# Kernel optimization log

Measured on AMD Instinct MI355X. Metric: run time of the kernel, lower is better.

## Reference

```python
import jax, jax.numpy as jnp
import numpy as np

B, S, T, D = 4, 512, 512, 256


def setup_inputs() -> dict:
    key = jax.random.key(0)
    ks = jax.random.split(key, 10)
    scale = 1.0 / np.sqrt(D)
    return {
        "source": jax.random.normal(ks[0], (B, S, D), jnp.float32),
        "target": jax.random.normal(ks[1], (B, T, D), jnp.float32),
        "W_src": jax.random.uniform(ks[2], (D, D), jnp.float32, -scale, scale),
        "b_src": jax.random.uniform(ks[3], (D,), jnp.float32, -scale, scale),
        "W_tgt": jax.random.uniform(ks[4], (D, D), jnp.float32, -scale, scale),
        "b_tgt": jax.random.uniform(ks[5], (D,), jnp.float32, -scale, scale),
        "W_res": jax.random.uniform(ks[6], (D, 1), jnp.float32, -scale, scale),
        "b_res": jax.random.uniform(ks[7], (1,), jnp.float32, -scale, scale),
        "W_prob": jax.random.uniform(ks[8], (D, 2), jnp.float32, -scale, scale),
        "b_prob": jax.random.uniform(ks[9], (2,), jnp.float32, -scale, scale),
    }


def reference(source, target, W_src, b_src, W_tgt, b_tgt, W_res, b_res, W_prob, b_prob):
    # source: (B,S,D), target: (B,T,D)
    src_lin = jnp.einsum("bsd,de->bse", source, W_src) + b_src  # (B,S,D)
    tgt_lin = jnp.einsum("btd,de->bte", target, W_tgt) + b_tgt  # (B,T,D)
    # Bahdanau-style additive attention: (B,T,S,D) broadcast, tanh, D->1
    h = jnp.tanh(src_lin[:, None, :, :] + tgt_lin[:, :, None, :])  # (B,T,S,D)
    genP = jnp.einsum("btsd,d->bts", h, W_res[:, 0]) + b_res[0]     # (B,T,S)
    prob = jax.nn.softmax(jnp.einsum("btd,de->bte", target, W_prob) + b_prob, axis=-1)  # (B,T,2)
    return genP, prob
```

## Files before the change

### kernel.cpp

```cpp
#include <hip/hip_runtime.h>

#define B_ 4
#define S_ 512
#define T_ 512
#define D_ 256
#define NSRC (B_ * S_)
#define NROW 4096
#define K2F 2.8853900817779268f

typedef __attribute__((ext_vector_type(8))) short short8;
typedef __attribute__((ext_vector_type(4))) float f32x4;
typedef __attribute__((ext_vector_type(2))) float f32x2;

__device__ __forceinline__ unsigned short f2bf(float f) {
    union { float f; unsigned u; } v; v.f = f;
    unsigned r = v.u + 0x7FFF + ((v.u >> 16) & 1);
    return (unsigned short)(r >> 16);
}

__global__ __launch_bounds__(256) void ysyt_kernel(
    const float* __restrict__ src, const float* __restrict__ tgt,
    const float* __restrict__ Wsrc, const float* __restrict__ Wtgt,
    const float* __restrict__ Wp,  const float* __restrict__ bp,
    const float* __restrict__ bsrc, const float* __restrict__ btgt,
    float* __restrict__ yst, float* __restrict__ out)
{
    __shared__ unsigned short lwt[16384];
    const int bid = blockIdx.x, tid = threadIdx.x;
    const int lane = tid & 63, w = tid >> 6;

    if (bid < 256) {
        const int rowblk = bid >> 2, colq = bid & 3;
        const int R0 = rowblk * 64;
        const int n = lane & 15, quad = lane >> 4;
        const int mat = (R0 >= NSRC) ? 1 : 0;
        const float* bias = mat ? btgt : bsrc;
        const float* Wm = mat ? Wtgt : Wsrc;
        const float* xb = mat ? &tgt[(R0 - NSRC) * D_] : &src[R0 * D_];

        {
            const int r = tid;
            const int ksr = r >> 5, qr = (r >> 3) & 3, jr = r & 7;
            const int wbase = ksr * 512 + qr * 8 + jr;
            #pragma unroll 4
            for (int i = 0; i < 16; i++) {
                float4 v = *(const float4*)&Wm[r * D_ + colq * 64 + 4 * i];
                const int cc = 4 * i;
                lwt[((cc + 0) >> 4) * 4096 + ((cc + 0) & 15) * 32 + wbase] = f2bf(v.x);
                lwt[((cc + 1) >> 4) * 4096 + ((cc + 1) & 15) * 32 + wbase] = f2bf(v.y);
                lwt[((cc + 2) >> 4) * 4096 + ((cc + 2) & 15) * 32 + wbase] = f2bf(v.z);
                lwt[((cc + 3) >> 4) * 4096 + ((cc + 3) & 15) * 32 + wbase] = f2bf(v.w);
            }
        }

        short8 af[8];
        #pragma unroll
        for (int ks = 0; ks < 8; ks++) {
            const float* p = &xb[(w * 16 + n) * D_ + ks * 32 + quad * 8];
            float4 u0 = *(const float4*)p;
            float4 u1 = *(const float4*)(p + 4);
            short8 v;
            v[0] = (short)f2bf(u0.x); v[1] = (short)f2bf(u0.y);
            v[2] = (short)f2bf(u0.z); v[3] = (short)f2bf(u0.w);
            v[4] = (short)f2bf(u1.x); v[5] = (short)f2bf(u1.y);
            v[6] = (short)f2bf(u1.z); v[7] = (short)f2bf(u1.w);
            af[ks] = v;
        }
        __syncthreads();

        #pragma unroll
        for (int gc = 0; gc < 4; gc++) {
            const int gcol = colq * 4 + gc;
            const unsigned short* bp2 = &lwt[gc * 4096 + n * 32 + quad * 8];
            short8 bf[8];
            #pragma unroll
            for (int ks = 0; ks < 8; ks++) bf[ks] = *(const short8*)&bp2[ks * 512];
            f32x4 a4 = {0.f, 0.f, 0.f, 0.f};
            #pragma unroll
            for (int ks = 0; ks < 8; ks++)
                a4 = __builtin_amdgcn_mfma_f32_16x16x32_bf16(af[ks], bf[ks], a4, 0, 0, 0);
            const float bv = bias[gcol * 16 + n];
            float4 o;
            o.x = __builtin_amdgcn_exp2f((a4[0] + bv) * K2F);
            o.y = __builtin_amdgcn_exp2f((a4[1] + bv) * K2F);
            o.z = __builtin_amdgcn_exp2f((a4[2] + bv) * K2F);
            o.w = __builtin_amdgcn_exp2f((a4[3] + bv) * K2F);
            *(float4*)&yst[(gcol * 16 + n) * NROW + R0 + w * 16 + quad * 4] = o;
        }
    } else {
        int row  = (bid - 256) * 4 + w;
        float p0 = 0.f, p1 = 0.f;
        #pragma unroll
        for (int i = 0; i < 4; i++) {
            int d = lane + i * 64;
            float v = tgt[row * D_ + d];
            float2 wv = *(const float2*)&Wp[d * 2];
            p0 = fmaf(v, wv.x, p0);
            p1 = fmaf(v, wv.y, p1);
        }
        #pragma unroll
        for (int off = 32; off > 0; off >>= 1) {
            p0 += __shfl_down(p0, off, 64);
            p1 += __shfl_down(p1, off, 64);
        }
        if (lane == 0) {
            const float L2E = 1.4426950408889634f;
            float l0 = p0 + bp[0], l1 = p1 + bp[1];
            float e10 = __builtin_amdgcn_exp2f((l1 - l0) * L2E);
            float e01 = __builtin_amdgcn_exp2f((l0 - l1) * L2E);
            out[B_ * T_ * S_ + row * 2 + 0] = __builtin_amdgcn_rcpf(1.f + e10);
            out[B_ * T_ * S_ + row * 2 + 1] = __builtin_amdgcn_rcpf(1.f + e01);
        }
    }
}

__global__ __launch_bounds__(256) void genp_kernel(
    const float* __restrict__ yst,
    const float* __restrict__ Wres, const float* __restrict__ bres,
    float* __restrict__ out)
{
    const int tid = threadIdx.x;
    const int lane = tid & 63;
    const int s0 = blockIdx.x * 64;
    const int t0 = blockIdx.y * 32;
    const int b  = blockIdx.z >> 1;
    const int dh = blockIdx.z & 1;
    const int m  = tid & 15;
    const int g  = tid >> 4;

    const int scol = b * S_ + s0 + 4 * m;
    const int tcol = NSRC + b * T_ + t0 + 2 * g;
    const int dbase = dh * 128;

    f32x2 acc[2][2];
    acc[0][0] = (f32x2){0.f, 0.f}; acc[0][1] = (f32x2){0.f, 0.f};
    acc[1][0] = (f32x2){0.f, 0.f}; acc[1][1] = (f32x2){0.f, 0.f};
    const f32x2 one2 = {1.f, 1.f};

    #define KQLOAD(AS, AT, DQ) do {                                          \
        _Pragma("unroll")                                                    \
        for (int k = 0; k < 4; k++) {                                        \
            AS[k] = *(const float4*)&yst[(size_t)((DQ) + k) * NROW + scol];  \
            AT[k] = *(const float2*)&yst[(size_t)((DQ) + k) * NROW + tcol];  \
        }                                                                    \
    } while (0)

    #define KQBODY(AS, AT, DQ) do {                                          \
        const float w0 = Wres[(DQ) + 0], w1 = Wres[(DQ) + 1];                \
        const float w2 = Wres[(DQ) + 2], w3 = Wres[(DQ) + 3];                \
        const f32x2 wv0 = {w0, w0}, wv1 = {w1, w1};                          \
        const f32x2 wv2 = {w2, w2}, wv3 = {w3, w3};                          \
        _Pragma("unroll")                                                    \
        for (int i = 0; i < 2; i++) {                                        \
            const float c0 = i ? AT[0].y : AT[0].x;                          \
            const float c1 = i ? AT[1].y : AT[1].x;                          \
            const float c2 = i ? AT[2].y : AT[2].x;                          \
            const float c3 = i ? AT[3].y : AT[3].x;                          \
            const f32x2 c0v = {c0, c0}, c1v = {c1, c1};                      \
            const f32x2 c2v = {c2, c2}, c3v = {c3, c3};                      \
            _Pragma("unroll")                                                \
            for (int jp = 0; jp < 2; jp++) {                                 \
                const f32x2 a0 = jp ? (f32x2){AS[0].z, AS[0].w}              \
                                    : (f32x2){AS[0].x, AS[0].y};             \
                const f32x2 a1 = jp ? (f32x2){AS[1].z, AS[1].w}              \
                                    : (f32x2){AS[1].x, AS[1].y};             \
                const f32x2 a2 = jp ? (f32x2){AS[2].z, AS[2].w}              \
                                    : (f32x2){AS[2].x, AS[2].y};             \
                const f32x2 a3 = jp ? (f32x2){AS[3].z, AS[3].w}              \
                                    : (f32x2){AS[3].x, AS[3].y};             \
                f32x2 dd0 = a0 * c0v + one2;                                 \
                f32x2 dd1 = a1 * c1v + one2;                                 \
                f32x2 dd2 = a2 * c2v + one2;                                 \
                f32x2 dd3 = a3 * c3v + one2;                                 \
                f32x2 p01 = dd0 * dd1;                                       \
                f32x2 p23 = dd2 * dd3;                                       \
                f32x2 den = p01 * p23;                                       \
                f32x2 u01 = dd1 * wv0; u01 = dd0 * wv1 + u01;                \
                f32x2 u23 = dd3 * wv2; u23 = dd2 * wv3 + u23;                \
                f32x2 num = u01 * p23; num = u23 * p01 + num;                \
                f32x2 r;                                                     \
                r.x = __builtin_amdgcn_rcpf(den.x);                          \
                r.y = __builtin_amdgcn_rcpf(den.y);                          \
                acc[i][jp] = num * r + acc[i][jp];                           \
            }                                                                \
        }                                                                    \
    } while (0)

    float4 sA[4], sB[4];
    float2 tA[4], tB[4];
    KQLOAD(sA, tA, dbase);
    for (int it = 0; it < 16; it++) {
        const int dq = dbase + it * 8;
        KQLOAD(sB, tB, dq + 4);
        KQBODY(sA, tA, dq);
        if (it < 15) KQLOAD(sA, tA, dq + 8);
        KQBODY(sB, tB, dq + 4);
    }
    #undef KQLOAD
    #undef KQBODY

    float cw = Wres[lane] + Wres[lane + 64] + Wres[lane + 128] + Wres[lane + 192];
    #pragma unroll
    for (int off = 32; off > 0; off >>= 1) cw += __shfl_xor(cw, off, 64);
    const float C0 = (dh == 0) ? (cw + bres[0]) : 0.f;

    #pragma unroll
    for (int i = 0; i < 2; i++) {
        float* orow = &out[(size_t)(b * T_ + t0 + 2 * g + i) * S_ + s0 + 4 * m];
        #pragma unroll
        for (int jp = 0; jp < 2; jp++) {
            unsafeAtomicAdd(&orow[2 * jp + 0], C0 - 2.f * acc[i][jp].x);
            unsafeAtomicAdd(&orow[2 * jp + 1], C0 - 2.f * acc[i][jp].y);
        }
    }
}

extern "C" void kernel_launch(void* const* d_in, const int* in_sizes, int n_in,
                              void* d_out, int out_size, void* d_ws, size_t ws_size,
                              hipStream_t stream) {
    const float* source = (const float*)d_in[0];
    const float* target = (const float*)d_in[1];
    const float* W_src  = (const float*)d_in[2];
    const float* b_src  = (const float*)d_in[3];
    const float* W_tgt  = (const float*)d_in[4];
    const float* b_tgt  = (const float*)d_in[5];
    const float* W_res  = (const float*)d_in[6];
    const float* b_res  = (const float*)d_in[7];
    const float* W_prob = (const float*)d_in[8];
    const float* b_prob = (const float*)d_in[9];
    float* out = (float*)d_out;

    float* yst = (float*)d_ws;

    ysyt_kernel<<<768, 256, 0, stream>>>(source, target, W_src, W_tgt,
                                         W_prob, b_prob, b_src, b_tgt,
                                         yst, out);
    genp_kernel<<<dim3(8, 16, 8), 256, 0, stream>>>(yst, W_res, b_res, out);
}
```

Measured before the change: 130.2 us.

## Stage ys/yt tiles in LDS and enlarge per-thread output tile in genp

genp_kernel now loads 64x64 slices of the source and target projections into shared memory once per block and computes a 4x4 output tile per thread from LDS. The d dimension is split four ways instead of two, and the t tile grows to 64. This targets repeated global/L2 reads of the projection data and raises arithmetic per load. In exchange it doubles the number of atomic adds to the output and adds a block-level barrier and LDS traffic.

```diff
diff --git a/kernel.cpp b/kernel.cpp
--- a/kernel.cpp
+++ b/kernel.cpp
@@ -119,55 +119,70 @@
     const float* __restrict__ Wres, const float* __restrict__ bres,
     float* __restrict__ out)
 {
+    __shared__ float lys[64][68];
+    __shared__ float lyt[64][68];
+
     const int tid = threadIdx.x;
     const int lane = tid & 63;
     const int s0 = blockIdx.x * 64;
-    const int t0 = blockIdx.y * 32;
-    const int b  = blockIdx.z >> 1;
-    const int dh = blockIdx.z & 1;
+    const int t0 = blockIdx.y * 64;
+    const int b  = blockIdx.z >> 2;
+    const int dq = blockIdx.z & 3;
+    const int d0 = dq * 64;
     const int m  = tid & 15;
     const int g  = tid >> 4;
 
-    const int scol = b * S_ + s0 + 4 * m;
-    const int tcol = NSRC + b * T_ + t0 + 2 * g;
-    const int dbase = dh * 128;
-
-    f32x2 acc[2][2];
-    acc[0][0] = (f32x2){0.f, 0.f}; acc[0][1] = (f32x2){0.f, 0.f};
-    acc[1][0] = (f32x2){0.f, 0.f}; acc[1][1] = (f32x2){0.f, 0.f};
+    {
+        const int r = tid >> 2, q = tid & 3;
+        const int sbase = b * S_ + s0;
+        const int tbase = NSRC + b * T_ + t0;
+        #pragma unroll
+        for (int j = 0; j < 4; j++) {
+            float4 vs = *(const float4*)&yst[(size_t)(d0 + r) * NROW + sbase + q * 16 + 4 * j];
+            float4 vt = *(const float4*)&yst[(size_t)(d0 + r) * NROW + tbase + q * 16 + 4 * j];
+            *(float4*)&lys[r][q * 16 + 4 * j] = vs;
+            *(float4*)&lyt[r][q * 16 + 4 * j] = vt;
+        }
+    }
+    __syncthreads();
+
+    f32x2 acc[4][2];
+    #pragma unroll
+    for (int i = 0; i < 4; i++) {
+        acc[i][0] = (f32x2){0.f, 0.f};
+        acc[i][1] = (f32x2){0.f, 0.f};
+    }
     const f32x2 one2 = {1.f, 1.f};
 
-    #define KQLOAD(AS, AT, DQ) do {                                          \
-        _Pragma("unroll")                                                    \
-        for (int k = 0; k < 4; k++) {                                        \
-            AS[k] = *(const float4*)&yst[(size_t)((DQ) + k) * NROW + scol];  \
-            AT[k] = *(const float2*)&yst[(size_t)((DQ) + k) * NROW + tcol];  \
-        }                                                                    \
-    } while (0)
-
-    #define KQBODY(AS, AT, DQ) do {                                          \
-        const float w0 = Wres[(DQ) + 0], w1 = Wres[(DQ) + 1];                \
-        const float w2 = Wres[(DQ) + 2], w3 = Wres[(DQ) + 3];                \
-        const f32x2 wv0 = {w0, w0}, wv1 = {w1, w1};                          \
-        const f32x2 wv2 = {w2, w2}, wv3 = {w3, w3};                          \
-        _Pragma("unroll")                                                    \
-        for (int i = 0; i < 2; i++) {                                        \
-            const float c0 = i ? AT[0].y : AT[0].x;                          \
-            const float c1 = i ? AT[1].y : AT[1].x;                          \
-            const float c2 = i ? AT[2].y : AT[2].x;                          \
-            const float c3 = i ? AT[3].y : AT[3].x;                          \
-            const f32x2 c0v = {c0, c0}, c1v = {c1, c1};                      \
-            const f32x2 c2v = {c2, c2}, c3v = {c3, c3};                      \
+    #pragma unroll 4
+    for (int kq = 0; kq < 16; kq++) {
+        const int dk = 4 * kq;
+        float4 sA[4], tA[4];
+        #pragma unroll
+        for (int k = 0; k < 4; k++) {
+            sA[k] = *(const float4*)&lys[dk + k][4 * m];
+            tA[k] = *(const float4*)&lyt[dk + k][4 * g];
+        }
+        const float w0 = Wres[d0 + dk + 0], w1 = Wres[d0 + dk + 1];
+        const float w2 = Wres[d0 + dk + 2], w3 = Wres[d0 + dk + 3];
+        const f32x2 wv0 = {w0, w0}, wv1 = {w1, w1};
+        const f32x2 wv2 = {w2, w2}, wv3 = {w3, w3};
+
+        #define FOLD(TT, COMP) {                                             \
+            const f32x2 c0v = {tA[0].COMP, tA[0].COMP};                      \
+            const f32x2 c1v = {tA[1].COMP, tA[1].COMP};                      \
+            const f32x2 c2v = {tA[2].COMP, tA[2].COMP};                      \
+            const f32x2 c3v = {tA[3].COMP, tA[3].COMP};                      \
             _Pragma("unroll")                                                \
             for (int jp = 0; jp < 2; jp++) {                                 \
-                const f32x2 a0 = jp ? (f32x2){AS[0].z, AS[0].w}              \
-                                    : (f32x2){AS[0].x, AS[0].y};             \
-                const f32x2 a1 = jp ? (f32x2){AS[1].z, AS[1].w}              \
-                                    : (f32x2){AS[1].x, AS[1].y};             \
-                const f32x2 a2 = jp ? (f32x2){AS[2].z, AS[2].w}              \
-                                    : (f32x2){AS[2].x, AS[2].y};             \
-                const f32x2 a3 = jp ? (f32x2){AS[3].z, AS[3].w}              \
-                                    : (f32x2){AS[3].x, AS[3].y};             \
+                const f32x2 a0 = jp ? (f32x2){sA[0].z, sA[0].w}              \
+                                    : (f32x2){sA[0].x, sA[0].y};             \
+                const f32x2 a1 = jp ? (f32x2){sA[1].z, sA[1].w}              \
+                                    : (f32x2){sA[1].x, sA[1].y};             \
+                const f32x2 a2 = jp ? (f32x2){sA[2].z, sA[2].w}              \
+                                    : (f32x2){sA[2].x, sA[2].y};             \
+                const f32x2 a3 = jp ? (f32x2){sA[3].z, sA[3].w}              \
+                                    : (f32x2){sA[3].x, sA[3].y};             \
                 f32x2 dd0 = a0 * c0v + one2;                                 \
                 f32x2 dd1 = a1 * c1v + one2;                                 \
                 f32x2 dd2 = a2 * c2v + one2;                                 \
@@ -181,37 +196,25 @@
                 f32x2 r;                                                     \
                 r.x = __builtin_amdgcn_rcpf(den.x);                          \
                 r.y = __builtin_amdgcn_rcpf(den.y);                          \
-                acc[i][jp] = num * r + acc[i][jp];                           \
+                acc[TT][jp] = num * r + acc[TT][jp];                         \
             }                                                                \
-        }                                                                    \
-    } while (0)
-
-    float4 sA[4], sB[4];
-    float2 tA[4], tB[4];
-    KQLOAD(sA, tA, dbase);
-    for (int it = 0; it < 16; it++) {
-        const int dq = dbase + it * 8;
-        KQLOAD(sB, tB, dq + 4);
-        KQBODY(sA, tA, dq);
-        if (it < 15) KQLOAD(sA, tA, dq + 8);
-        KQBODY(sB, tB, dq + 4);
-    }
-    #undef KQLOAD
-    #undef KQBODY
+        }
+        FOLD(0, x) FOLD(1, y) FOLD(2, z) FOLD(3, w)
+        #undef FOLD
+    }
 
     float cw = Wres[lane] + Wres[lane + 64] + Wres[lane + 128] + Wres[lane + 192];
     #pragma unroll
     for (int off = 32; off > 0; off >>= 1) cw += __shfl_xor(cw, off, 64);
-    const float C0 = (dh == 0) ? (cw + bres[0]) : 0.f;
+    const float C0 = (dq == 0) ? (cw + bres[0]) : 0.f;
 
     #pragma unroll
-    for (int i = 0; i < 2; i++) {
-        float* orow = &out[(size_t)(b * T_ + t0 + 2 * g + i) * S_ + s0 + 4 * m];
-        #pragma unroll
-        for (int jp = 0; jp < 2; jp++) {
-            unsafeAtomicAdd(&orow[2 * jp + 0], C0 - 2.f * acc[i][jp].x);
-            unsafeAtomicAdd(&orow[2 * jp + 1], C0 - 2.f * acc[i][jp].y);
-        }
+    for (int i = 0; i < 4; i++) {
+        float* orow = &out[(size_t)(b * T_ + t0 + 4 * g + i) * S_ + s0 + 4 * m];
+        unsafeAtomicAdd(&orow[0], C0 - 2.f * acc[i][0].x);
+        unsafeAtomicAdd(&orow[1], C0 - 2.f * acc[i][0].y);
+        unsafeAtomicAdd(&orow[2], C0 - 2.f * acc[i][1].x);
+        unsafeAtomicAdd(&orow[3], C0 - 2.f * acc[i][1].y);
     }
 }
 
@@ -235,5 +238,5 @@
     ysyt_kernel<<<768, 256, 0, stream>>>(source, target, W_src, W_tgt,
                                          W_prob, b_prob, b_src, b_tgt,
                                          yst, out);
-    genp_kernel<<<dim3(8, 16, 8), 256, 0, stream>>>(yst, W_res, b_res, out);
-}
+    genp_kernel<<<dim3(8, 8, 16), 256, 0, stream>>>(yst, W_res, b_res, out);
+}
```

New measurement: 147.6 us. +13.4%, slower.
